# Kernel optimization log

Measured on AMD Instinct MI355X. Metric: run time of the kernel, lower is better.

Reference implementation:

```python
import jax, jax.numpy as jnp
jax.config.update("jax_enable_x64", True)
import numpy as np

B, IN_DIM, OUT_DIM = 65536, 256, 256
SCALE = 100.0


def setup_inputs() -> dict:
    key = jax.random.key(0)
    k1, k2, k3 = jax.random.split(key, 3)
    c_x = jax.random.randint(k1, (B, IN_DIM), 0, 200, dtype=jnp.int64)
    weight = jax.random.normal(k2, (OUT_DIM, IN_DIM), dtype=jnp.float32)
    true_bias = jax.random.normal(k3, (OUT_DIM,), dtype=jnp.float32)
    in_scale = jnp.ones((1,), dtype=jnp.float32) * jnp.float32(SCALE)
    return {"c_x": c_x, "weight": weight, "true_bias": true_bias, "in_scale": in_scale}


def scale_round(x, scale):
    # torch.round(x * scale).long()
    return jnp.round(x * scale).astype(jnp.int64)


def reference(c_x, weight, true_bias, in_scale):
    scale = jnp.float32(SCALE)
    s = in_scale[0]
    # quantize weight (done in __init__ in the original) and bias (done per-forward)
    w_q = scale_round(weight, scale)                 # [OUT, IN] int64
    b_q = scale_round(true_bias, s * scale)          # [OUT] int64
    # fhe.matrix_product(W, x.T).T == x @ W.T, then add_matrix_vector adds bias per row
    out = jnp.matmul(c_x, w_q.T) + b_q[None, :]      # [B, OUT] int64
    return out, s * scale
```

## Files before the change

### kernel.cpp

```cpp
#include <hip/hip_runtime.h>

typedef _Float16 half8 __attribute__((ext_vector_type(8)));
typedef _Float16 half4 __attribute__((ext_vector_type(4)));
typedef float floatx4 __attribute__((ext_vector_type(4)));

#define IN_DIM 256
#define OUT_DIM 256
#define M_TILE 64
#define ROWSTR 264

__global__ void quant_kernel(const float* __restrict__ w,
                             const float* __restrict__ bias,
                             const float* __restrict__ in_scale,
                             _Float16* __restrict__ wqp,
                             float* __restrict__ bq,
                             float* __restrict__ out_scalar) {
    int t = blockIdx.x * blockDim.x + threadIdx.x;
    if (t < (OUT_DIM * IN_DIM) / 8) {
        int lane = t & 63;
        int ks   = (t >> 6) & 7;
        int ct   = t >> 9;
        int row  = ct * 16 + (lane & 15);
        int k0   = ks * 32 + (lane >> 4) * 8;
        const float* src = w + row * IN_DIM + k0;
        half8 h;
#pragma unroll
        for (int e = 0; e < 8; ++e)
            h[e] = (_Float16)rintf(src[e] * 100.0f);
        *((half8*)wqp + t) = h;
    }
    if (t < OUT_DIM) {
        float s2 = in_scale[0] * 100.0f;
        bq[t] = rintf(bias[t] * s2);
    }
    if (t == 0 && out_scalar != nullptr)
        out_scalar[0] = in_scale[0] * 100.0f;
}

__global__ __launch_bounds__(256, 4) void gemm_kernel(const int* __restrict__ cx,
                                                      const _Float16* __restrict__ wqp,
                                                      const float* __restrict__ bq,
                                                      float* __restrict__ out) {
    __shared__ _Float16 cT[M_TILE * ROWSTR];

    const int t = threadIdx.x;
    const size_t m0 = (size_t)blockIdx.x * M_TILE;

    const int* cbase = cx + m0 * IN_DIM;
#pragma unroll
    for (int i = 0; i < 16; ++i) {
        int flat = i * 1024 + t * 4;
        int4 v = *(const int4*)(cbase + flat);
        int row = flat >> 8;
        int col = flat & 255;
        half4 h;
        h.x = (_Float16)v.x; h.y = (_Float16)v.y;
        h.z = (_Float16)v.z; h.w = (_Float16)v.w;
        *(half4*)&cT[row * ROWSTR + col] = h;
    }
    __syncthreads();

    const int wave = t >> 6;
    const int lane = t & 63;
    const int m16  = lane & 15;
    const int quad = lane >> 4;

    floatx4 acc[4][4] = {};

    const half8* wbase = (const half8*)wqp;
#pragma unroll
    for (int ks = 0; ks < 8; ++ks) {
        half8 afr[4], bfr[4];
#pragma unroll
        for (int i = 0; i < 4; ++i)
            afr[i] = wbase[((wave * 4 + i) * 8 + ks) * 64 + lane];
        const int kb = ks * 32 + quad * 8;
#pragma unroll
        for (int j = 0; j < 4; ++j)
            bfr[j] = *(const half8*)&cT[(j * 16 + m16) * ROWSTR + kb];
#pragma unroll
        for (int i = 0; i < 4; ++i)
#pragma unroll
            for (int j = 0; j < 4; ++j)
                acc[i][j] = __builtin_amdgcn_mfma_f32_16x16x32_f16(afr[i], bfr[j], acc[i][j], 0, 0, 0);
    }

#pragma unroll
    for (int i = 0; i < 4; ++i) {
        int col = wave * 64 + i * 16 + quad * 4;
        floatx4 bv = *(const floatx4*)(bq + col);
#pragma unroll
        for (int j = 0; j < 4; ++j) {
            size_t row = m0 + j * 16 + m16;
            floatx4 v = acc[i][j] + bv;
            *(floatx4*)(out + row * OUT_DIM + col) = v;
        }
    }
}

extern "C" void kernel_launch(void* const* d_in, const int* in_sizes, int n_in,
                              void* d_out, int out_size, void* d_ws, size_t ws_size,
                              hipStream_t stream) {
    const int*   cx       = (const int*)d_in[0];
    const float* w        = (const float*)d_in[1];
    const float* bias     = (const float*)d_in[2];
    const float* in_scale = (const float*)d_in[3];
    float* out = (float*)d_out;

    _Float16* wqp = (_Float16*)d_ws;
    float*    bq  = (float*)((char*)d_ws + OUT_DIM * IN_DIM * 2);

    const int rows = in_sizes[0] / IN_DIM;
    const size_t gemm_elems = (size_t)rows * OUT_DIM;
    float* out_scalar = ((size_t)out_size > gemm_elems) ? (out + gemm_elems) : nullptr;

    quant_kernel<<<32, 256, 0, stream>>>(w, bias, in_scale, wqp, bq, out_scalar);
    gemm_kernel<<<rows / M_TILE, 256, 0, stream>>>(cx, wqp, bq, out);
}
```

Measured before the change: 123.9 us.

## Drop LDS staging; each wave loads its own 16 input rows into registers

```diff
diff --git a/kernel.cpp b/kernel.cpp
--- a/kernel.cpp
+++ b/kernel.cpp
@@ -1,13 +1,10 @@
 #include <hip/hip_runtime.h>
 
 typedef _Float16 half8 __attribute__((ext_vector_type(8)));
-typedef _Float16 half4 __attribute__((ext_vector_type(4)));
 typedef float floatx4 __attribute__((ext_vector_type(4)));
 
 #define IN_DIM 256
 #define OUT_DIM 256
-#define M_TILE 64
-#define ROWSTR 264
 
 __global__ void quant_kernel(const float* __restrict__ w,
                              const float* __restrict__ bias,
@@ -37,64 +34,45 @@
         out_scalar[0] = in_scale[0] * 100.0f;
 }
 
-__global__ __launch_bounds__(256, 4) void gemm_kernel(const int* __restrict__ cx,
+__global__ __launch_bounds__(256, 3) void gemm_kernel(const int* __restrict__ cx,
                                                       const _Float16* __restrict__ wqp,
                                                       const float* __restrict__ bq,
                                                       float* __restrict__ out) {
-    __shared__ _Float16 cT[M_TILE * ROWSTR];
-
-    const int t = threadIdx.x;
-    const size_t m0 = (size_t)blockIdx.x * M_TILE;
-
-    const int* cbase = cx + m0 * IN_DIM;
-#pragma unroll
-    for (int i = 0; i < 16; ++i) {
-        int flat = i * 1024 + t * 4;
-        int4 v = *(const int4*)(cbase + flat);
-        int row = flat >> 8;
-        int col = flat & 255;
-        half4 h;
-        h.x = (_Float16)v.x; h.y = (_Float16)v.y;
-        h.z = (_Float16)v.z; h.w = (_Float16)v.w;
-        *(half4*)&cT[row * ROWSTR + col] = h;
-    }
-    __syncthreads();
-
+    const int t    = threadIdx.x;
     const int wave = t >> 6;
     const int lane = t & 63;
     const int m16  = lane & 15;
     const int quad = lane >> 4;
 
-    floatx4 acc[4][4] = {};
+    const size_t row = (size_t)blockIdx.x * 64 + wave * 16 + m16;
+    const int* crow = cx + row * IN_DIM;
 
+    floatx4 acc[16] = {};
     const half8* wbase = (const half8*)wqp;
+
 #pragma unroll
     for (int ks = 0; ks < 8; ++ks) {
-        half8 afr[4], bfr[4];
+        const int* cp = crow + ks * 32 + quad * 8;
+        int4 c0 = *(const int4*)(cp);
+        int4 c1 = *(const int4*)(cp + 4);
+        half8 b;
+        b[0] = (_Float16)(float)c0.x; b[1] = (_Float16)(float)c0.y;
+        b[2] = (_Float16)(float)c0.z; b[3] = (_Float16)(float)c0.w;
+        b[4] = (_Float16)(float)c1.x; b[5] = (_Float16)(float)c1.y;
+        b[6] = (_Float16)(float)c1.z; b[7] = (_Float16)(float)c1.w;
 #pragma unroll
-        for (int i = 0; i < 4; ++i)
-            afr[i] = wbase[((wave * 4 + i) * 8 + ks) * 64 + lane];
-        const int kb = ks * 32 + quad * 8;
-#pragma unroll
-        for (int j = 0; j < 4; ++j)
-            bfr[j] = *(const half8*)&cT[(j * 16 + m16) * ROWSTR + kb];
-#pragma unroll
-        for (int i = 0; i < 4; ++i)
-#pragma unroll
-            for (int j = 0; j < 4; ++j)
-                acc[i][j] = __builtin_amdgcn_mfma_f32_16x16x32_f16(afr[i], bfr[j], acc[i][j], 0, 0, 0);
+        for (int ct = 0; ct < 16; ++ct) {
+            half8 a = wbase[(ct * 8 + ks) * 64 + lane];
+            acc[ct] = __builtin_amdgcn_mfma_f32_16x16x32_f16(a, b, acc[ct], 0, 0, 0);
+        }
     }
 
+    float* orow = out + row * OUT_DIM;
 #pragma unroll
-    for (int i = 0; i < 4; ++i) {
-        int col = wave * 64 + i * 16 + quad * 4;
+    for (int ct = 0; ct < 16; ++ct) {
+        int col = ct * 16 + quad * 4;
         floatx4 bv = *(const floatx4*)(bq + col);
-#pragma unroll
-        for (int j = 0; j < 4; ++j) {
-            size_t row = m0 + j * 16 + m16;
-            floatx4 v = acc[i][j] + bv;
-            *(floatx4*)(out + row * OUT_DIM + col) = v;
-        }
+        *(floatx4*)(orow + col) = acc[ct] + bv;
     }
 }
 
@@ -115,5 +93,5 @@
     float* out_scalar = ((size_t)out_size > gemm_elems) ? (out + gemm_elems) : nullptr;
 
     quant_kernel<<<32, 256, 0, stream>>>(w, bias, in_scale, wqp, bq, out_scalar);
-    gemm_kernel<<<rows / M_TILE, 256, 0, stream>>>(cx, wqp, bq, out);
+    gemm_kernel<<<rows / 64, 256, 0, stream>>>(cx, wqp, bq, out);
 }
```

Measured after the change: 176.0 us. 1.42x slower.

## Process two row tiles per block with register-prefetched second tile

Applied to the files above, without the earlier changes.

```diff
diff --git a/kernel.cpp b/kernel.cpp
--- a/kernel.cpp
+++ b/kernel.cpp
@@ -6,7 +6,6 @@
 
 #define IN_DIM 256
 #define OUT_DIM 256
-#define M_TILE 64
 #define ROWSTR 264
 
 __global__ void quant_kernel(const float* __restrict__ w,
@@ -37,16 +36,9 @@
         out_scalar[0] = in_scale[0] * 100.0f;
 }
 
-__global__ __launch_bounds__(256, 4) void gemm_kernel(const int* __restrict__ cx,
-                                                      const _Float16* __restrict__ wqp,
-                                                      const float* __restrict__ bq,
-                                                      float* __restrict__ out) {
-    __shared__ _Float16 cT[M_TILE * ROWSTR];
 
-    const int t = threadIdx.x;
-    const size_t m0 = (size_t)blockIdx.x * M_TILE;
-
-    const int* cbase = cx + m0 * IN_DIM;
+__device__ __forceinline__ void stage_tile(const int* __restrict__ cbase, int t,
+                                           _Float16* __restrict__ buf) {
 #pragma unroll
     for (int i = 0; i < 16; ++i) {
         int flat = i * 1024 + t * 4;
@@ -56,35 +48,36 @@
         half4 h;
         h.x = (_Float16)v.x; h.y = (_Float16)v.y;
         h.z = (_Float16)v.z; h.w = (_Float16)v.w;
-        *(half4*)&cT[row * ROWSTR + col] = h;
+        *(half4*)&buf[row * ROWSTR + col] = h;
     }
-    __syncthreads();
+}
 
-    const int wave = t >> 6;
-    const int lane = t & 63;
-    const int m16  = lane & 15;
-    const int quad = lane >> 4;
-
-    floatx4 acc[4][4] = {};
-
-    const half8* wbase = (const half8*)wqp;
+__device__ __forceinline__ void compute_tile(const _Float16* __restrict__ buf,
+                                             const half8* __restrict__ wbase,
+                                             int wave, int m16, int quad,
+                                             floatx4 (&acc)[4][4]) {
 #pragma unroll
     for (int ks = 0; ks < 8; ++ks) {
         half8 afr[4], bfr[4];
 #pragma unroll
         for (int i = 0; i < 4; ++i)
-            afr[i] = wbase[((wave * 4 + i) * 8 + ks) * 64 + lane];
+            afr[i] = wbase[((wave * 4 + i) * 8 + ks) * 64 + (quad * 16 + m16)];
         const int kb = ks * 32 + quad * 8;
 #pragma unroll
         for (int j = 0; j < 4; ++j)
-            bfr[j] = *(const half8*)&cT[(j * 16 + m16) * ROWSTR + kb];
+            bfr[j] = *(const half8*)&buf[(j * 16 + m16) * ROWSTR + kb];
 #pragma unroll
         for (int i = 0; i < 4; ++i)
 #pragma unroll
             for (int j = 0; j < 4; ++j)
                 acc[i][j] = __builtin_amdgcn_mfma_f32_16x16x32_f16(afr[i], bfr[j], acc[i][j], 0, 0, 0);
     }
+}
 
+__device__ __forceinline__ void store_tile(float* __restrict__ out, size_t m0,
+                                           const float* __restrict__ bq,
+                                           int wave, int m16, int quad,
+                                           floatx4 (&acc)[4][4]) {
 #pragma unroll
     for (int i = 0; i < 4; ++i) {
         int col = wave * 64 + i * 16 + quad * 4;
@@ -92,10 +85,58 @@
 #pragma unroll
         for (int j = 0; j < 4; ++j) {
             size_t row = m0 + j * 16 + m16;
-            floatx4 v = acc[i][j] + bv;
-            *(floatx4*)(out + row * OUT_DIM + col) = v;
+            *(floatx4*)(out + row * OUT_DIM + col) = acc[i][j] + bv;
         }
     }
+}
+
+__global__ __launch_bounds__(256, 2) void gemm_kernel(const int* __restrict__ cx,
+                                                      const _Float16* __restrict__ wqp,
+                                                      const float* __restrict__ bq,
+                                                      float* __restrict__ out) {
+    __shared__ _Float16 buf0[64 * ROWSTR];
+    __shared__ _Float16 buf1[64 * ROWSTR];
+
+    const int t    = threadIdx.x;
+    const int wave = t >> 6;
+    const int lane = t & 63;
+    const int m16  = lane & 15;
+    const int quad = lane >> 4;
+
+    const size_t m0   = (size_t)blockIdx.x * 128;
+    const int* cbase0 = cx + m0 * IN_DIM;
+    const int* cbase1 = cbase0 + 64 * IN_DIM;
+    const half8* wbase = (const half8*)wqp;
+
+    stage_tile(cbase0, t, buf0);
+    __syncthreads();
+
+    int4 creg[16];
+#pragma unroll
+    for (int i = 0; i < 16; ++i)
+        creg[i] = *(const int4*)(cbase1 + i * 1024 + t * 4);
+
+    floatx4 acc0[4][4] = {};
+    compute_tile(buf0, wbase, wave, m16, quad, acc0);
+
+#pragma unroll
+    for (int i = 0; i < 16; ++i) {
+        int flat = i * 1024 + t * 4;
+        int row = flat >> 8;
+        int col = flat & 255;
+        half4 h;
+        h.x = (_Float16)creg[i].x; h.y = (_Float16)creg[i].y;
+        h.z = (_Float16)creg[i].z; h.w = (_Float16)creg[i].w;
+        *(half4*)&buf1[row * ROWSTR + col] = h;
+    }
+
+    store_tile(out, m0, bq, wave, m16, quad, acc0);
+
+    __syncthreads();
+
+    floatx4 acc1[4][4] = {};
+    compute_tile(buf1, wbase, wave, m16, quad, acc1);
+    store_tile(out, m0 + 64, bq, wave, m16, quad, acc1);
 }
 
 extern "C" void kernel_launch(void* const* d_in, const int* in_sizes, int n_in,
@@ -115,5 +156,5 @@
     float* out_scalar = ((size_t)out_size > gemm_elems) ? (out + gemm_elems) : nullptr;
 
     quant_kernel<<<32, 256, 0, stream>>>(w, bias, in_scale, wqp, bq, out_scalar);
-    gemm_kernel<<<rows / M_TILE, 256, 0, stream>>>(cx, wqp, bq, out);
+    gemm_kernel<<<rows / 128, 256, 0, stream>>>(cx, wqp, bq, out);
 }
```

After: 128.5 us. 1.04x slower.
